# Kernel tuning notes

Hardware: AMD Instinct MI355X
Metric: run time of the kernel (lower is better)

The kernel has to match this reference:

```python
import jax, jax.numpy as jnp
import numpy as np

H = 1024      # hidden_size
NH = 16       # num_attention_heads
HD = H // NH  # attention_head_size = 64
FF = 4096     # intermediate_size
EPS = 1e-5


def setup_inputs() -> dict:
    key = jax.random.key(0)
    ks = jax.random.split(key, 16)
    B, S = 8, 512
    s = lambda d: 1.0 / np.sqrt(d)
    return {
        "hidden_states": jax.random.normal(ks[0], (B, S, H), jnp.float32),
        "attention_mask": jnp.zeros((B, 1, 1, S), jnp.float32),  # additive mask
        "wq": jax.random.normal(ks[1], (H, H), jnp.float32) * s(H),
        "bq": jnp.zeros((H,), jnp.float32),
        "wk": jax.random.normal(ks[2], (H, H), jnp.float32) * s(H),
        "bk": jnp.zeros((H,), jnp.float32),
        "wv": jax.random.normal(ks[3], (H, H), jnp.float32) * s(H),
        "bv": jnp.zeros((H,), jnp.float32),
        "wo": jax.random.normal(ks[4], (H, H), jnp.float32) * s(H),
        "bo": jnp.zeros((H,), jnp.float32),
        "ln1_g": jnp.ones((H,), jnp.float32),
        "ln1_b": jnp.zeros((H,), jnp.float32),
        "wi": jax.random.normal(ks[5], (H, FF), jnp.float32) * s(H),
        "bi": jnp.zeros((FF,), jnp.float32),
        "wo2": jax.random.normal(ks[6], (FF, H), jnp.float32) * s(FF),
        "bo2": jnp.zeros((H,), jnp.float32),
        "ln2_g": jnp.ones((H,), jnp.float32),
        "ln2_b": jnp.zeros((H,), jnp.float32),
    }


def _layer_norm(x, g, b):
    mu = jnp.mean(x, axis=-1, keepdims=True)
    var = jnp.mean(jnp.square(x - mu), axis=-1, keepdims=True)
    return (x - mu) * jax.lax.rsqrt(var + EPS) * g + b


def reference(hidden_states, attention_mask, wq, bq, wk, bk, wv, bv,
              wo, bo, ln1_g, ln1_b, wi, bi, wo2, bo2, ln2_g, ln2_b):
    B, S, _ = hidden_states.shape
    split = lambda x: x.reshape(B, S, NH, HD).transpose(0, 2, 1, 3)  # [B,NH,S,HD]
    q = split(hidden_states @ wq + bq)
    k = split(hidden_states @ wk + bk)
    v = split(hidden_states @ wv + bv)
    # scaled dot-product attention with additive mask (dropout = eval identity)
    scores = jnp.einsum("bhqd,bhkd->bhqk", q, k) / np.sqrt(HD)
    scores = scores + attention_mask
    probs = jax.nn.softmax(scores, axis=-1)
    ctx = jnp.einsum("bhqk,bhkd->bhqd", probs, v)
    ctx = ctx.transpose(0, 2, 1, 3).reshape(B, S, H)
    # RobertaSelfOutput: dense + residual + LayerNorm
    attn_out = _layer_norm(ctx @ wo + bo + hidden_states, ln1_g, ln1_b)
    # FFN: intermediate (gelu) + output dense + residual + LayerNorm
    inter = jax.nn.gelu(attn_out @ wi + bi, approximate=False)
    layer_out = _layer_norm(inter @ wo2 + bo2 + attn_out, ln2_g, ln2_b)
    return layer_out
```

## Files before the change

kernel.cpp:

```cpp
#include <hip/hip_runtime.h>
#include <math.h>

#define DI __device__ __forceinline__

typedef unsigned short u16;
typedef __attribute__((ext_vector_type(8))) u16 u16x8;
typedef __attribute__((ext_vector_type(4))) u16 u16x4;
typedef __attribute__((ext_vector_type(8))) __bf16 bf16x8;
typedef __attribute__((ext_vector_type(4))) float f32x4;

typedef const __attribute__((address_space(1))) unsigned int g_u32;
typedef __attribute__((address_space(3))) unsigned int l_u32;

DI float bf2f(u16 u) {
  unsigned v = ((unsigned)u) << 16;
  float f; __builtin_memcpy(&f, &v, 4); return f;
}
DI u16 f2bf(float f) {
  unsigned u; __builtin_memcpy(&u, &f, 4);
  u += 0x7fff + ((u >> 16) & 1);
  return (u16)(u >> 16);
}
DI f32x4 mfma16(bf16x8 a, bf16x8 b, f32x4 c) {
  return __builtin_amdgcn_mfma_f32_16x16x32_bf16(a, b, c, 0, 0, 0);
}
DI void gl16(const void* g, const u16* lds) {
  __builtin_amdgcn_global_load_lds((g_u32*)g, (l_u32*)lds, 16, 0, 0);
}

__global__ __launch_bounds__(256) void cvt_bf16_k(const float* __restrict__ in,
                                                  u16* __restrict__ out, int n) {
  int i = (blockIdx.x * 256 + threadIdx.x) * 8;
  if (i >= n) return;
  float4 a = *(const float4*)(in + i);
  float4 b = *(const float4*)(in + i + 4);
  u16x8 o;
  o[0] = f2bf(a.x); o[1] = f2bf(a.y); o[2] = f2bf(a.z); o[3] = f2bf(a.w);
  o[4] = f2bf(b.x); o[5] = f2bf(b.y); o[6] = f2bf(b.z); o[7] = f2bf(b.w);
  *(u16x8*)(out + i) = o;
}

__global__ __launch_bounds__(256) void tcvt_k(const float* __restrict__ in,
                                              u16* __restrict__ out, int K, int N) {
  __shared__ float tile[32][33];
  int n0 = blockIdx.x * 32, k0 = blockIdx.y * 32;
  int tx = threadIdx.x & 31, ty = threadIdx.x >> 5;
  #pragma unroll
  for (int i = 0; i < 4; i++) {
    int kr = ty + i * 8;
    tile[kr][tx] = in[(size_t)(k0 + kr) * N + n0 + tx];
  }
  __syncthreads();
  #pragma unroll
  for (int i = 0; i < 4; i++) {
    int nr = ty + i * 8;
    out[(size_t)(n0 + nr) * K + k0 + tx] = f2bf(tile[tx][nr]);
  }
}

__global__ __launch_bounds__(256) void pack_bias_k(const float* __restrict__ b0,
                                                   const float* __restrict__ b1,
                                                   const float* __restrict__ b2,
                                                   float* __restrict__ out) {
  int i = blockIdx.x * 256 + threadIdx.x;
  float v = (i < 1024) ? b0[i] : (i < 2048 ? b1[i - 1024] : b2[i - 2048]);
  out[i] = v;
}

#define QUAD(d, mh, nh) do {                                                          \
  const u16* Ab_ = &sA[d][wr][0];                                                     \
  const u16* Bb_ = &sB[d][wc >> 1][0];                                                \
  bf16x8 af_[4][2], bv_[2][2];                                                        \
  _Pragma("unroll") for (int i_ = 0; i_ < 4; i_++) {                                  \
    int row_ = (mh) * 64 + i_ * 16 + r15;                                             \
    _Pragma("unroll") for (int ks_ = 0; ks_ < 2; ks_++)                               \
      af_[i_][ks_] = *(const bf16x8*)&Ab_[row_ * 64 + ((((ks_ << 2) | kg) + row_) & 7) * 8]; } \
  _Pragma("unroll") for (int j_ = 0; j_ < 2; j_++) {                                  \
    int row_ = (wc & 1) * 64 + (nh) * 32 + j_ * 16 + r15;                             \
    _Pragma("unroll") for (int ks_ = 0; ks_ < 2; ks_++)                               \
      bv_[j_][ks_] = *(const bf16x8*)&Bb_[row_ * 64 + ((((ks_ << 2) | kg) + row_) & 7) * 8]; } \
  __builtin_amdgcn_s_barrier();                                                       \
  __builtin_amdgcn_s_setprio(1);                                                      \
  _Pragma("unroll") for (int i_ = 0; i_ < 4; i_++)                                    \
    _Pragma("unroll") for (int j_ = 0; j_ < 2; j_++)                                  \
      _Pragma("unroll") for (int ks_ = 0; ks_ < 2; ks_++)                             \
        acc[(mh) * 4 + i_][(nh) * 2 + j_] =                                           \
            mfma16(af_[i_][ks_], bv_[j_][ks_], acc[(mh) * 4 + i_][(nh) * 2 + j_]);    \
  __builtin_amdgcn_s_setprio(0);                                                      \
} while (0)

template<int EPI, int SPLITK>
__global__ __launch_bounds__(512, 2) void gemm8p_k(const u16* __restrict__ A,
                                                   const u16* __restrict__ Bt,
                                                   const float* __restrict__ bias,
                                                   void* __restrict__ out,
                                                   int M, int N, int K) {
  __shared__ __align__(16) u16 sA[2][2][128 * 64];
  __shared__ __align__(16) u16 sB[2][2][128 * 64];
  const int tid = threadIdx.x;
  const int lane = tid & 63, wid = tid >> 6;
  const int wr = wid >> 2, wc = wid & 3;
  const int r15 = lane & 15, kg = lane >> 4;

  const int GX = gridDim.x, GY = gridDim.y;
  int nwg = GX * GY;
  int orig = blockIdx.y * GX + blockIdx.x;
  int s = (orig & 7) * (nwg >> 3) + (orig >> 3);
  int bx = s / GY, by = s - bx * GY;
  const int bm = by * 256, bn = bx * 256;

  const int z = blockIdx.z;
  int tilesK = K >> 6;
  int qs = tilesK / SPLITK, rs = tilesK - qs * SPLITK;
  int ntz = qs + (z < rs ? 1 : 0);
  int k0 = (z * qs + (z < rs ? z : rs)) << 6;

  f32x4 acc[8][4];
  #pragma unroll
  for (int i = 0; i < 8; i++)
    #pragma unroll
    for (int j = 0; j < 4; j++) acc[i][j] = (f32x4){0.f, 0.f, 0.f, 0.f};

  auto stageHalf = [&](const u16* __restrict__ X, int grow0, int kcol, u16* dst) {
    #pragma unroll
    for (int s2 = 0; s2 < 2; s2++) {
      int idx = (s2 << 9) | tid;
      int drow = idx >> 3;
      int gslot = (idx - drow) & 7;
      gl16(X + (size_t)(grow0 + drow) * K + kcol + (gslot << 3),
           dst + (((s2 << 9) | (wid << 6)) << 3));
    }
  };

  stageHalf(A,  bm,       k0, &sA[0][0][0]);
  stageHalf(Bt, bn,       k0, &sB[0][0][0]);
  stageHalf(A,  bm + 128, k0, &sA[0][1][0]);
  stageHalf(Bt, bn + 128, k0, &sB[0][1][0]);

  for (int t = 0; t < ntz; ++t) {
    int d = t & 1;
    asm volatile("s_waitcnt vmcnt(0)" ::: "memory");
    __builtin_amdgcn_s_barrier();
    const bool pf = (t + 1 < ntz);
    const int kn = k0 + ((t + 1) << 6);
    if (pf) { stageHalf(A, bm,        kn, &sA[d ^ 1][0][0]);
              stageHalf(Bt, bn,       kn, &sB[d ^ 1][0][0]); }
    QUAD(d, 0, 0);
    if (pf) { stageHalf(A, bm + 128,  kn, &sA[d ^ 1][1][0]);
              stageHalf(Bt, bn + 128, kn, &sB[d ^ 1][1][0]); }
    QUAD(d, 0, 1);
    QUAD(d, 1, 0);
    QUAD(d, 1, 1);
    asm volatile("s_waitcnt lgkmcnt(0)" ::: "memory");
    __builtin_amdgcn_sched_barrier(0);
  }

  #pragma unroll
  for (int ii = 0; ii < 8; ii++) {
    int row = bm + wr * 128 + ii * 16 + kg * 4;
    #pragma unroll
    for (int jj = 0; jj < 4; jj++) {
      int col = bn + wc * 64 + jj * 16 + r15;
      if (EPI == 4) {
        size_t zoff = (size_t)z * M * N;
        #pragma unroll
        for (int q2 = 0; q2 < 4; q2++)
          ((float*)out)[zoff + (size_t)(row + q2) * N + col] = acc[ii][jj][q2];
      } else {
        float bv = bias[col];
        #pragma unroll
        for (int q2 = 0; q2 < 4; q2++) {
          float v = acc[ii][jj][q2] + bv;
          if (EPI == 2) v = 0.5f * v * (1.0f + erff(v * 0.70710678118f));
          ((u16*)out)[(size_t)(row + q2) * N + col] = f2bf(v);
        }
      }
    }
  }
}

template<int EPI>
__global__ __launch_bounds__(256) void gemm_bt_k(const u16* __restrict__ A,
                                                 const u16* __restrict__ Bt,
                                                 const float* __restrict__ bias,
                                                 const void* __restrict__ resid,
                                                 u16* __restrict__ out,
                                                 int M, int N, int K) {
  __shared__ __align__(16) u16 As[2][128 * 64];
  __shared__ __align__(16) u16 Bs[2][128 * 64];
  const int tid = threadIdx.x;
  const int lane = tid & 63, wid = tid >> 6;
  const int wm = (wid >> 1) * 64, wn = (wid & 1) * 64;
  const int r15 = lane & 15, kg = lane >> 4;
  const int srow = lane >> 3;
  const int scolb = (lane & 7) << 4;

  const int GX = gridDim.x, GY = gridDim.y;
  int nwg = GX * GY;
  int orig = blockIdx.y * GX + blockIdx.x;
  int s = (orig & 7) * (nwg >> 3) + (orig >> 3);
  int bx = s / GY, by = s - bx * GY;
  const int bm = by * 128, bn = bx * 128;

  f32x4 acc[4][4];
  #pragma unroll
  for (int i = 0; i < 4; i++)
    #pragma unroll
    for (int j = 0; j < 4; j++) acc[i][j] = (f32x4){0.f, 0.f, 0.f, 0.f};

  auto STAGE = [&](int buf, int kt) {
    #pragma unroll
    for (int c = 0; c < 4; c++) {
      int chunk = (c << 2) | wid;
      int row = (chunk << 3) + srow;
      gl16((const char*)A + ((size_t)(bm + row) * K + kt) * 2 + scolb,
           &As[buf][chunk << 9]);
      gl16((const char*)Bt + ((size_t)(bn + row) * K + kt) * 2 + scolb,
           &Bs[buf][chunk << 9]);
    }
  };
  auto COMPUTE = [&](int buf) {
    #pragma unroll
    for (int ks = 0; ks < 2; ks++) {
      bf16x8 af[4], bfr[4];
      #pragma unroll
      for (int i = 0; i < 4; i++)
        af[i] = *(const bf16x8*)&As[buf][(wm + i * 16 + r15) * 64 + ks * 32 + kg * 8];
      #pragma unroll
      for (int i = 0; i < 4; i++)
        bfr[i] = *(const bf16x8*)&Bs[buf][(wn + i * 16 + r15) * 64 + ks * 32 + kg * 8];
      #pragma unroll
      for (int i = 0; i < 4; i++)
        #pragma unroll
        for (int j = 0; j < 4; j++)
          acc[i][j] = mfma16(af[i], bfr[j], acc[i][j]);
    }
  };

  const int nt = K >> 6;
  STAGE(0, 0);
  __syncthreads();
  int cur = 0;
  for (int t = 0; t + 1 < nt; ++t) {
    STAGE(cur ^ 1, (t + 1) << 6);
    COMPUTE(cur);
    __syncthreads();
    cur ^= 1;
  }
  COMPUTE(cur);

  #pragma unroll
  for (int i = 0; i < 4; i++) {
    int row0 = bm + wm + i * 16 + kg * 4;
    #pragma unroll
    for (int j = 0; j < 4; j++) {
      int col = bn + wn + j * 16 + r15;
      float bv = bias[col];
      #pragma unroll
      for (int q2 = 0; q2 < 4; q2++) {
        int row = row0 + q2;
        float v = acc[i][j][q2] + bv;
        if (EPI == 1) v += ((const float*)resid)[(size_t)row * N + col];
        out[(size_t)row * N + col] = f2bf(v);
      }
    }
  }
}

__global__ __launch_bounds__(256) void attn_k(const u16* __restrict__ QKV,
                                              const float* __restrict__ mask,
                                              u16* __restrict__ ctx) {
  __shared__ __align__(16) u16 sQ[32 * 72];
  __shared__ __align__(16) u16 sK[64 * 72];
  __shared__ __align__(16) u16 sVt[64 * 72];
  __shared__ __align__(16) u16 sS[32 * 520];
  __shared__ float sSum[32];
  const int t = threadIdx.x, lane = t & 63, wid = t >> 6;
  const int qb = blockIdx.x, h = blockIdx.y, b = blockIdx.z;
  const int r15 = lane & 15, kg = lane >> 4;
  const int mg = wid >> 1, half = wid & 1;
  const size_t qoff = (size_t)h * 64;
  const size_t koff = 1024 + qoff, voff = 2048 + qoff;

  {
    int row = t >> 3, d0 = (t & 7) * 8;
    *(u16x8*)&sQ[row * 72 + d0] =
        *(const u16x8*)&QKV[((size_t)(b * 512 + qb * 32 + row)) * 3072 + qoff + d0];
  }

  for (int kt = 0; kt < 8; ++kt) {
    int row = t >> 2, d0 = (t & 3) * 16;
    const u16* src = &QKV[((size_t)(b * 512 + kt * 64 + row)) * 3072 + koff + d0];
    *(u16x8*)&sK[row * 72 + d0] = *(const u16x8*)src;
    *(u16x8*)&sK[row * 72 + d0 + 8] = *(const u16x8*)(src + 8);
    __syncthreads();
    bf16x8 qf0 = *(const bf16x8*)&sQ[(mg * 16 + r15) * 72 + kg * 8];
    bf16x8 qf1 = *(const bf16x8*)&sQ[(mg * 16 + r15) * 72 + 32 + kg * 8];
    #pragma unroll
    for (int n2 = 0; n2 < 2; n2++) {
      int nt = half * 2 + n2;
      f32x4 sacc = (f32x4){0.f, 0.f, 0.f, 0.f};
      sacc = mfma16(qf0, *(const bf16x8*)&sK[(nt * 16 + r15) * 72 + kg * 8], sacc);
      sacc = mfma16(qf1, *(const bf16x8*)&sK[(nt * 16 + r15) * 72 + 32 + kg * 8], sacc);
      int col = kt * 64 + nt * 16 + r15;
      float mv = mask[b * 512 + col];
      #pragma unroll
      for (int q = 0; q < 4; q++) {
        int rl = mg * 16 + kg * 4 + q;
        sS[rl * 520 + col] = f2bf(sacc[q] * 0.125f + mv);
      }
    }
    __syncthreads();
  }

  {
    int row = t >> 3, seg = t & 7;
    float mx = -1e30f;
    for (int j = 0; j < 64; j++)
      mx = fmaxf(mx, bf2f(sS[row * 520 + seg * 64 + j]));
    mx = fmaxf(mx, __shfl_xor(mx, 1));
    mx = fmaxf(mx, __shfl_xor(mx, 2));
    mx = fmaxf(mx, __shfl_xor(mx, 4));
    float sum = 0.f;
    for (int j = 0; j < 64; j++) {
      int idx = row * 520 + seg * 64 + j;
      float p = __expf(bf2f(sS[idx]) - mx);
      sum += p;
      sS[idx] = f2bf(p);
    }
    sum += __shfl_xor(sum, 1);
    sum += __shfl_xor(sum, 2);
    sum += __shfl_xor(sum, 4);
    if (seg == 0) sSum[row] = sum;
  }
  __syncthreads();

  f32x4 pacc[2];
  pacc[0] = (f32x4){0.f, 0.f, 0.f, 0.f};
  pacc[1] = (f32x4){0.f, 0.f, 0.f, 0.f};
  for (int vt = 0; vt < 8; ++vt) {
    int rowk = t >> 2, d0 = (t & 3) * 16;
    const u16* src = &QKV[((size_t)(b * 512 + vt * 64 + rowk)) * 3072 + voff + d0];
    u16x8 v0 = *(const u16x8*)src;
    u16x8 v1 = *(const u16x8*)(src + 8);
    #pragma unroll
    for (int e = 0; e < 8; e++) {
      sVt[(d0 + e) * 72 + rowk] = v0[e];
      sVt[(d0 + 8 + e) * 72 + rowk] = v1[e];
    }
    __syncthreads();
    bf16x8 pf0 = *(const bf16x8*)&sS[(mg * 16 + r15) * 520 + vt * 64 + kg * 8];
    bf16x8 pf1 = *(const bf16x8*)&sS[(mg * 16 + r15) * 520 + vt * 64 + 32 + kg * 8];
    #pragma unroll
    for (int n2 = 0; n2 < 2; n2++) {
      int dcol = half * 32 + n2 * 16;
      pacc[n2] = mfma16(pf0, *(const bf16x8*)&sVt[(dcol + r15) * 72 + kg * 8], pacc[n2]);
      pacc[n2] = mfma16(pf1, *(const bf16x8*)&sVt[(dcol + r15) * 72 + 32 + kg * 8], pacc[n2]);
    }
    __syncthreads();
  }
  #pragma unroll
  for (int n2 = 0; n2 < 2; n2++) {
    int d = half * 32 + n2 * 16 + r15;
    #pragma unroll
    for (int q = 0; q < 4; q++) {
      int rl = mg * 16 + kg * 4 + q;
      float v = pacc[n2][q] / sSum[rl];
      ctx[((size_t)(b * 512 + qb * 32 + rl)) * 1024 + qoff + d] = f2bf(v);
    }
  }
}

template<int OUTF32>
__global__ __launch_bounds__(256) void ln_k(const u16* __restrict__ in,
                                            const float* __restrict__ g,
                                            const float* __restrict__ be,
                                            void* __restrict__ out) {
  int row = blockIdx.x, t = threadIdx.x;
  const u16* rp = in + (size_t)row * 1024 + t * 4;
  u16x4 raw = *(const u16x4*)rp;
  float x[4];
  #pragma unroll
  for (int i = 0; i < 4; i++) x[i] = bf2f(raw[i]);
  float s = x[0] + x[1] + x[2] + x[3];
  float q = x[0]*x[0] + x[1]*x[1] + x[2]*x[2] + x[3]*x[3];
  #pragma unroll
  for (int off = 32; off; off >>= 1) {
    s += __shfl_down(s, off);
    q += __shfl_down(q, off);
  }
  __shared__ float rs_[4], rq_[4];
  int wid = t >> 6, lane = t & 63;
  if (!lane) { rs_[wid] = s; rq_[wid] = q; }
  __syncthreads();
  float S1 = rs_[0] + rs_[1] + rs_[2] + rs_[3];
  float S2 = rq_[0] + rq_[1] + rq_[2] + rq_[3];
  float mu = S1 * (1.0f / 1024.0f);
  float inv = rsqrtf(S2 * (1.0f / 1024.0f) - mu * mu + 1e-5f);
  #pragma unroll
  for (int i = 0; i < 4; i++) {
    int c = t * 4 + i;
    float y = (x[i] - mu) * inv * g[c] + be[c];
    if (OUTF32) ((float*)out)[(size_t)row * 1024 + c] = y;
    else        ((u16*)out)[(size_t)row * 1024 + c] = f2bf(y);
  }
}

__global__ __launch_bounds__(256) void ln2r_k(const float* __restrict__ part,
                                              const float* __restrict__ bias,
                                              const u16* __restrict__ resid,
                                              const float* __restrict__ g,
                                              const float* __restrict__ be,
                                              float* __restrict__ out) {
  const int row = blockIdx.x, t = threadIdx.x;
  const size_t base = (size_t)row * 1024 + t * 4;
  float4 p0 = *(const float4*)(part + base);
  float4 p1 = *(const float4*)(part + 4194304 + base);
  float4 p2 = *(const float4*)(part + 8388608 + base);
  u16x4 rr = *(const u16x4*)(resid + base);
  float x[4];
  x[0] = p0.x + p1.x + p2.x + bias[t*4+0] + bf2f(rr[0]);
  x[1] = p0.y + p1.y + p2.y + bias[t*4+1] + bf2f(rr[1]);
  x[2] = p0.z + p1.z + p2.z + bias[t*4+2] + bf2f(rr[2]);
  x[3] = p0.w + p1.w + p2.w + bias[t*4+3] + bf2f(rr[3]);
  float s = x[0] + x[1] + x[2] + x[3];
  float q = x[0]*x[0] + x[1]*x[1] + x[2]*x[2] + x[3]*x[3];
  #pragma unroll
  for (int off = 32; off; off >>= 1) {
    s += __shfl_down(s, off);
    q += __shfl_down(q, off);
  }
  __shared__ float rs_[4], rq_[4];
  int wid = t >> 6, lane = t & 63;
  if (!lane) { rs_[wid] = s; rq_[wid] = q; }
  __syncthreads();
  float S1 = rs_[0] + rs_[1] + rs_[2] + rs_[3];
  float S2 = rq_[0] + rq_[1] + rq_[2] + rq_[3];
  float mu = S1 * (1.0f / 1024.0f);
  float inv = rsqrtf(S2 * (1.0f / 1024.0f) - mu * mu + 1e-5f);
  #pragma unroll
  for (int i = 0; i < 4; i++) {
    int c = t * 4 + i;
    out[(size_t)row * 1024 + c] = (x[i] - mu) * inv * g[c] + be[c];
  }
}

extern "C" void kernel_launch(void* const* d_in, const int* in_sizes, int n_in,
                              void* d_out, int out_size, void* d_ws, size_t ws_size,
                              hipStream_t stream) {
  const float* hidden = (const float*)d_in[0];
  const float* mask   = (const float*)d_in[1];
  const float* wq  = (const float*)d_in[2];  const float* bq  = (const float*)d_in[3];
  const float* wk  = (const float*)d_in[4];  const float* bk  = (const float*)d_in[5];
  const float* wv  = (const float*)d_in[6];  const float* bv  = (const float*)d_in[7];
  const float* wo  = (const float*)d_in[8];  const float* bo  = (const float*)d_in[9];
  const float* ln1g = (const float*)d_in[10]; const float* ln1b = (const float*)d_in[11];
  const float* wi  = (const float*)d_in[12]; const float* bi  = (const float*)d_in[13];
  const float* wo2 = (const float*)d_in[14]; const float* bo2 = (const float*)d_in[15];
  const float* ln2g = (const float*)d_in[16]; const float* ln2b = (const float*)d_in[17];

  char* ws = (char*)d_ws;
  u16*   WqkvT = (u16*)(ws + 0);
  u16*   WoT   = (u16*)(ws + 6291456);
  u16*   Xb    = (u16*)(ws + 8388608);
  u16*   QKVb  = (u16*)(ws + 16777216);
  u16*   Ctx   = (u16*)(ws + 41943040);
  u16*   AD    = (u16*)(ws + 50331648);
  float* part  = (float*)(ws + 0);
  u16*   AO    = (u16*)(ws + 58720256);
  u16*   Inter = (u16*)(ws + 67108864);
  u16*   WiT   = (u16*)(ws + 100663296);
  u16*   Wo2T  = (u16*)(ws + 109051904);
  float* bqkv  = (float*)(ws + 117440512);

  cvt_bf16_k<<<2048, 256, 0, stream>>>(hidden, Xb, 4194304);
  tcvt_k<<<dim3(32, 32),  256, 0, stream>>>(wq,  WqkvT,                1024, 1024);
  tcvt_k<<<dim3(32, 32),  256, 0, stream>>>(wk,  WqkvT + 1024 * 1024,  1024, 1024);
  tcvt_k<<<dim3(32, 32),  256, 0, stream>>>(wv,  WqkvT + 2048 * 1024,  1024, 1024);
  tcvt_k<<<dim3(32, 32),  256, 0, stream>>>(wo,  WoT,  1024, 1024);
  tcvt_k<<<dim3(128, 32), 256, 0, stream>>>(wi,  WiT,  1024, 4096);
  tcvt_k<<<dim3(32, 128), 256, 0, stream>>>(wo2, Wo2T, 4096, 1024);
  pack_bias_k<<<12, 256, 0, stream>>>(bq, bk, bv, bqkv);

  gemm8p_k<0, 1><<<dim3(12, 16, 1), 512, 0, stream>>>(Xb, WqkvT, bqkv, QKVb, 4096, 3072, 1024);

  attn_k<<<dim3(16, 16, 8), 256, 0, stream>>>(QKVb, mask, Ctx);

  gemm_bt_k<1><<<dim3(8, 32), 256, 0, stream>>>(Ctx, WoT, bo, hidden, AD, 4096, 1024, 1024);
  ln_k<0><<<4096, 256, 0, stream>>>(AD, ln1g, ln1b, AO);

  gemm8p_k<2, 1><<<dim3(16, 16, 1), 512, 0, stream>>>(AO, WiT, bi, Inter, 4096, 4096, 1024);

  gemm8p_k<4, 3><<<dim3(4, 16, 3), 512, 0, stream>>>(Inter, Wo2T, nullptr, part, 4096, 1024, 4096);

  ln2r_k<<<4096, 256, 0, stream>>>(part, bo2, AO, ln2g, ln2b, (float*)d_out);
}
```

Baseline: 433.6 us.

## Prefetch two tiles ahead with partial vmcnt waits and swizzle small-GEMM LDS

Both GEMM kernels now issue global-to-LDS loads two k-tiles ahead and wait with vmcnt(8), so only the older tile must have landed before compute. The refill of a buffer moves after a second barrier that follows compute, which keeps loads in flight across the whole iteration. Global pointers are precomputed and advanced incrementally to cut address arithmetic. The small 128x128 kernel also gains an XOR-style rotated LDS layout to reduce bank conflicts on fragment reads. The cost is an extra barrier per iteration and reliance on exact counts of outstanding loads.

```diff
diff --git a/kernel.cpp b/kernel.cpp
--- a/kernel.cpp
+++ b/kernel.cpp
@@ -121,38 +121,40 @@
     #pragma unroll
     for (int j = 0; j < 4; j++) acc[i][j] = (f32x4){0.f, 0.f, 0.f, 0.f};
 
-  auto stageHalf = [&](const u16* __restrict__ X, int grow0, int kcol, u16* dst) {
-    #pragma unroll
-    for (int s2 = 0; s2 < 2; s2++) {
-      int idx = (s2 << 9) | tid;
-      int drow = idx >> 3;
-      int gslot = (idx - drow) & 7;
-      gl16(X + (size_t)(grow0 + drow) * K + kcol + (gslot << 3),
-           dst + (((s2 << 9) | (wid << 6)) << 3));
-    }
+  const int drw = tid >> 3;
+  const int gsl8 = ((tid - drw) & 7) << 3;
+  const u16* pA0 = A  + (size_t)(bm +       drw) * K + k0 + gsl8;
+  const u16* pA1 = A  + (size_t)(bm + 128 + drw) * K + k0 + gsl8;
+  const u16* pB0 = Bt + (size_t)(bn +       drw) * K + k0 + gsl8;
+  const u16* pB1 = Bt + (size_t)(bn + 128 + drw) * K + k0 + gsl8;
+  const size_t s2o = (size_t)64 * K;
+  const int dld = wid << 9;
+
+  auto stageTile = [&](int d) {
+    u16* dA0 = &sA[d][0][dld]; u16* dA1 = &sA[d][1][dld];
+    u16* dB0 = &sB[d][0][dld]; u16* dB1 = &sB[d][1][dld];
+    gl16(pA0, dA0); gl16(pA0 + s2o, dA0 + 4096);
+    gl16(pB0, dB0); gl16(pB0 + s2o, dB0 + 4096);
+    gl16(pA1, dA1); gl16(pA1 + s2o, dA1 + 4096);
+    gl16(pB1, dB1); gl16(pB1 + s2o, dB1 + 4096);
+    pA0 += 64; pA1 += 64; pB0 += 64; pB1 += 64;
   };
 
-  stageHalf(A,  bm,       k0, &sA[0][0][0]);
-  stageHalf(Bt, bn,       k0, &sB[0][0][0]);
-  stageHalf(A,  bm + 128, k0, &sA[0][1][0]);
-  stageHalf(Bt, bn + 128, k0, &sB[0][1][0]);
+  stageTile(0);
+  if (ntz > 1) stageTile(1);
 
   for (int t = 0; t < ntz; ++t) {
     int d = t & 1;
-    asm volatile("s_waitcnt vmcnt(0)" ::: "memory");
+    if (t + 1 < ntz) asm volatile("s_waitcnt vmcnt(8)" ::: "memory");
+    else             asm volatile("s_waitcnt vmcnt(0)" ::: "memory");
     __builtin_amdgcn_s_barrier();
-    const bool pf = (t + 1 < ntz);
-    const int kn = k0 + ((t + 1) << 6);
-    if (pf) { stageHalf(A, bm,        kn, &sA[d ^ 1][0][0]);
-              stageHalf(Bt, bn,       kn, &sB[d ^ 1][0][0]); }
     QUAD(d, 0, 0);
-    if (pf) { stageHalf(A, bm + 128,  kn, &sA[d ^ 1][1][0]);
-              stageHalf(Bt, bn + 128, kn, &sB[d ^ 1][1][0]); }
     QUAD(d, 0, 1);
     QUAD(d, 1, 0);
     QUAD(d, 1, 1);
-    asm volatile("s_waitcnt lgkmcnt(0)" ::: "memory");
+    __builtin_amdgcn_s_barrier();
     __builtin_amdgcn_sched_barrier(0);
+    if (t + 2 < ntz) stageTile(d);
   }
 
   #pragma unroll
@@ -193,7 +195,6 @@
   const int wm = (wid >> 1) * 64, wn = (wid & 1) * 64;
   const int r15 = lane & 15, kg = lane >> 4;
   const int srow = lane >> 3;
-  const int scolb = (lane & 7) << 4;
 
   const int GX = gridDim.x, GY = gridDim.y;
   int nwg = GX * GY;
@@ -208,15 +209,21 @@
     #pragma unroll
     for (int j = 0; j < 4; j++) acc[i][j] = (f32x4){0.f, 0.f, 0.f, 0.f};
 
+  const u16* pAc[4]; const u16* pBc[4];
+  #pragma unroll
+  for (int c = 0; c < 4; c++) {
+    int chunk = (c << 2) | wid;
+    int row = (chunk << 3) + srow;
+    int gsl = ((lane & 7) - row) & 7;
+    pAc[c] = A  + (size_t)(bm + row) * K + (gsl << 3);
+    pBc[c] = Bt + (size_t)(bn + row) * K + (gsl << 3);
+  }
   auto STAGE = [&](int buf, int kt) {
     #pragma unroll
     for (int c = 0; c < 4; c++) {
       int chunk = (c << 2) | wid;
-      int row = (chunk << 3) + srow;
-      gl16((const char*)A + ((size_t)(bm + row) * K + kt) * 2 + scolb,
-           &As[buf][chunk << 9]);
-      gl16((const char*)Bt + ((size_t)(bn + row) * K + kt) * 2 + scolb,
-           &Bs[buf][chunk << 9]);
+      gl16(pAc[c] + kt, &As[buf][chunk << 9]);
+      gl16(pBc[c] + kt, &Bs[buf][chunk << 9]);
     }
   };
   auto COMPUTE = [&](int buf) {
@@ -224,11 +231,15 @@
     for (int ks = 0; ks < 2; ks++) {
       bf16x8 af[4], bfr[4];
       #pragma unroll
-      for (int i = 0; i < 4; i++)
-        af[i] = *(const bf16x8*)&As[buf][(wm + i * 16 + r15) * 64 + ks * 32 + kg * 8];
+      for (int i = 0; i < 4; i++) {
+        int row = wm + i * 16 + r15;
+        af[i] = *(const bf16x8*)&As[buf][row * 64 + (((ks << 2) + kg + row) & 7) * 8];
+      }
       #pragma unroll
-      for (int i = 0; i < 4; i++)
-        bfr[i] = *(const bf16x8*)&Bs[buf][(wn + i * 16 + r15) * 64 + ks * 32 + kg * 8];
+      for (int i = 0; i < 4; i++) {
+        int row = wn + i * 16 + r15;
+        bfr[i] = *(const bf16x8*)&Bs[buf][row * 64 + (((ks << 2) + kg + row) & 7) * 8];
+      }
       #pragma unroll
       for (int i = 0; i < 4; i++)
         #pragma unroll
@@ -239,15 +250,16 @@
 
   const int nt = K >> 6;
   STAGE(0, 0);
-  __syncthreads();
-  int cur = 0;
-  for (int t = 0; t + 1 < nt; ++t) {
-    STAGE(cur ^ 1, (t + 1) << 6);
-    COMPUTE(cur);
-    __syncthreads();
-    cur ^= 1;
-  }
-  COMPUTE(cur);
+  if (nt > 1) STAGE(1, 64);
+  for (int t = 0; t < nt; ++t) {
+    if (t + 1 < nt) asm volatile("s_waitcnt vmcnt(8)" ::: "memory");
+    else            asm volatile("s_waitcnt vmcnt(0)" ::: "memory");
+    __builtin_amdgcn_s_barrier();
+    COMPUTE(t & 1);
+    __builtin_amdgcn_s_barrier();
+    __builtin_amdgcn_sched_barrier(0);
+    if (t + 2 < nt) STAGE(t & 1, (t + 2) << 6);
+  }
 
   #pragma unroll
   for (int i = 0; i < 4; i++) {
```

After: 412.0 us. 5.0% less time.
